# Optimization experiments

Measured on AMD Instinct MI355X. Metric: run time of the kernel, lower is better.

## Reference

```python
import jax, jax.numpy as jnp
import numpy as np

B, D, H, T = 4096, 512, 1024, 20
DT = 0.05  # time spacing for the integration grid


def setup_inputs() -> dict:
    key = jax.random.key(0)
    k1, k2, k3 = jax.random.split(key, 3)
    x0 = jax.random.normal(k1, (B, D), dtype=jnp.float32)
    t = jnp.arange(T, dtype=jnp.float32) * DT  # monotonically increasing time grid
    W1 = jax.random.normal(k2, (D, H), dtype=jnp.float32) * (1.0 / np.sqrt(D))
    b1 = jnp.zeros((H,), dtype=jnp.float32)
    W2 = jax.random.normal(k3, (H, D), dtype=jnp.float32) * (1.0 / np.sqrt(H))
    b2 = jnp.zeros((D,), dtype=jnp.float32)
    return {"x0": x0, "t": t, "W1": W1, "b1": b1, "W2": W2, "b2": b2}


def reference(x0, t, W1, b1, W2, b2):
    """NeuralODE forward: integrate dy/dt = f(t, y) from x0 over grid t.

    f is the canonical 2-layer tanh MLP odefunc (autonomous in t, as in the
    typical odefunc(input_dim) construction). Integration uses classic RK4 on
    the supplied time grid (fixed-grid equivalent of odeint). Returns the
    trajectory with shape [T, B, D], matching torchdiffeq's odeint output.
    """

    def f(ti, y):  # odefunc: [B, D] -> [B, D]
        return jnp.tanh(y @ W1 + b1) @ W2 + b2

    def rk4_step(y, td):
        ti, dt = td
        half = dt * 0.5
        k1 = f(ti, y)
        k2 = f(ti + half, y + half * k1)
        k3 = f(ti + half, y + half * k2)
        k4 = f(ti + dt, y + dt * k3)
        y_next = y + (dt / 6.0) * (k1 + 2.0 * k2 + 2.0 * k3 + k4)
        return y_next, y_next

    dts = t[1:] - t[:-1]  # [T-1]
    _, ys = jax.lax.scan(rk4_step, x0, (t[:-1], dts))  # ys: [T-1, B, D]
    return jnp.concatenate([x0[None], ys], axis=0)  # [T, B, D]
```

## Files before the change

kernel.cpp:

```cpp
#include <hip/hip_runtime.h>
#include <hip/hip_bf16.h>
#include <cstdint>

#define BATCH 4096
#define DIM   512
#define HID   1024
#define TSTEPS 20

typedef unsigned short u16;
typedef short s16x8 __attribute__((ext_vector_type(8)));
typedef float f32x4 __attribute__((ext_vector_type(4)));

__device__ __forceinline__ u16 f2bf(float f) {
    unsigned int u = __float_as_uint(f);
    u = (u + 0x7FFFu + ((u >> 16) & 1u)) >> 16;
    return (u16)u;
}

__global__ void init_state(const float* __restrict__ x0, float* __restrict__ out0,
                           u16* __restrict__ ybf, int n) {
    int i = blockIdx.x * blockDim.x + threadIdx.x;
    if (i < n) { float v = x0[i]; out0[i] = v; ybf[i] = f2bf(v); }
}

__global__ void transpose_convert(const float* __restrict__ W, u16* __restrict__ Wt,
                                  int K, int N) {
    int n = blockIdx.x * 32 + threadIdx.x;
    int k = blockIdx.y * 8  + threadIdx.y;
    if (n < N && k < K) Wt[(size_t)n * K + k] = f2bf(W[(size_t)k * N + n]);
}

template<int BM, int BN, int EPI>
__global__ __launch_bounds__(256, 2) void gemm_bt(
    const u16* __restrict__ A,
    const u16* __restrict__ Bt,
    const float* __restrict__ bias,
    int M, int N, int K,
    u16* __restrict__ actOut,
    const float* __restrict__ ybase,
    float* __restrict__ ynext,
    float* __restrict__ accum,
    u16* __restrict__ ybf,
    const float* __restrict__ tgrid, int step)
{
    constexpr int AC = BM / 8;
    constexpr int BC = BN / 8;
    constexpr int CPW = (AC + BC) / 4;
    static_assert(CPW == 4 || CPW == 6, "vmcnt literals below assume 4 or 6");
    constexpr int WM = BM / 32;
    constexpr int WN = BN / 32;
    constexpr int BUFE = (BM + BN) * 64;

    __shared__ u16 lds[3 * BUFE];

    const int tid  = threadIdx.x;
    const int lane = tid & 63;
    const int wid  = tid >> 6;
    const int wy   = wid >> 1;
    const int wx   = wid & 1;
    const int brow = blockIdx.x * BM;
    const int bcol = blockIdx.y * BN;

    const int srow = lane >> 3;
    const int scol = ((lane & 7) ^ srow) * 8;

    f32x4 acc[WM][WN];
#pragma unroll
    for (int m = 0; m < WM; ++m)
#pragma unroll
        for (int n = 0; n < WN; ++n)
            acc[m][n] = (f32x4){0.f, 0.f, 0.f, 0.f};

    auto stage = [&](int buf, int kt) {
        const int k0 = kt * 64;
        u16* base = &lds[buf * BUFE];
#pragma unroll
        for (int c0 = 0; c0 < CPW; ++c0) {
            int c = wid * CPW + c0;
            if (c < AC) {
                int row = c * 8 + srow;
                const u16* g = A + (size_t)(brow + row) * K + k0 + scol;
                __builtin_amdgcn_global_load_lds(
                    (const __attribute__((address_space(1))) unsigned int*)g,
                    (__attribute__((address_space(3))) unsigned int*)&base[c * 512],
                    16, 0, 0);
            } else {
                int cb = c - AC;
                int row = cb * 8 + srow;
                const u16* g = Bt + (size_t)(bcol + row) * K + k0 + scol;
                __builtin_amdgcn_global_load_lds(
                    (const __attribute__((address_space(1))) unsigned int*)g,
                    (__attribute__((address_space(3))) unsigned int*)&base[BM * 64 + cb * 512],
                    16, 0, 0);
            }
        }
    };

    const int NT = K / 64;

    stage(0, 0);
    stage(1, 1);

    for (int kt = 0; kt < NT; ++kt) {
        if (kt < NT - 1) {
            if constexpr (CPW == 6) asm volatile("s_waitcnt vmcnt(6)" ::: "memory");
            else                    asm volatile("s_waitcnt vmcnt(4)" ::: "memory");
        } else {
            asm volatile("s_waitcnt vmcnt(0)" ::: "memory");
        }
        __builtin_amdgcn_s_barrier();

        const char* lb = (const char*)&lds[(kt % 3) * BUFE];

        s16x8 af[2][WM], bfr[2][WN];
#pragma unroll
        for (int ks = 0; ks < 2; ++ks) {
#pragma unroll
            for (int m = 0; m < WM; ++m) {
                int row = wy * (BM / 2) + m * 16 + (lane & 15);
                unsigned byte = (unsigned)(row * 128 + (ks * 32 + (lane >> 4) * 8) * 2);
                byte ^= (unsigned)((row & 7) << 4);
                af[ks][m] = *(const s16x8*)(lb + byte);
            }
#pragma unroll
            for (int n = 0; n < WN; ++n) {
                int row = wx * (BN / 2) + n * 16 + (lane & 15);
                unsigned byte = (unsigned)(BM * 128 + row * 128 + (ks * 32 + (lane >> 4) * 8) * 2);
                byte ^= (unsigned)((row & 7) << 4);
                bfr[ks][n] = *(const s16x8*)(lb + byte);
            }
        }

        if (kt + 2 < NT) stage((kt + 2) % 3, kt + 2);

#pragma unroll
        for (int ks = 0; ks < 2; ++ks)
#pragma unroll
            for (int m = 0; m < WM; ++m)
#pragma unroll
                for (int n = 0; n < WN; ++n)
                    acc[m][n] = __builtin_amdgcn_mfma_f32_16x16x32_bf16(
                        af[ks][m], bfr[ks][n], acc[m][n], 0, 0, 0);

        __builtin_amdgcn_s_barrier();
    }

    float dtv = 0.f;
    if constexpr (EPI >= 1) dtv = tgrid[step + 1] - tgrid[step];

#pragma unroll
    for (int m = 0; m < WM; ++m) {
        int row0 = brow + wy * (BM / 2) + m * 16 + (lane >> 4) * 4;
#pragma unroll
        for (int n = 0; n < WN; ++n) {
            int col = bcol + wx * (BN / 2) + n * 16 + (lane & 15);
            float bv = bias[col];
#pragma unroll
            for (int j = 0; j < 4; ++j) {
                int row = row0 + j;
                float v = acc[m][n][j] + bv;
                if constexpr (EPI == 0) {
                    actOut[(size_t)row * HID + col] = f2bf(tanhf(v));
                } else {
                    size_t idx = (size_t)row * DIM + col;
                    float yb = ybase[idx];
                    if constexpr (EPI == 1) {
                        accum[idx] = v;
                        ybf[idx] = f2bf(yb + 0.5f * dtv * v);
                    } else if constexpr (EPI == 2) {
                        accum[idx] += 2.0f * v;
                        ybf[idx] = f2bf(yb + 0.5f * dtv * v);
                    } else if constexpr (EPI == 3) {
                        accum[idx] += 2.0f * v;
                        ybf[idx] = f2bf(yb + dtv * v);
                    } else {
                        float yn = yb + (dtv * (1.0f / 6.0f)) * (accum[idx] + v);
                        ynext[idx] = yn;
                        ybf[idx] = f2bf(yn);
                    }
                }
            }
        }
    }
}

extern "C" void kernel_launch(void* const* d_in, const int* in_sizes, int n_in,
                              void* d_out, int out_size, void* d_ws, size_t ws_size,
                              hipStream_t stream) {
    (void)in_sizes; (void)n_in; (void)out_size; (void)ws_size;
    const float* x0 = (const float*)d_in[0];
    const float* t  = (const float*)d_in[1];
    const float* W1 = (const float*)d_in[2];
    const float* b1 = (const float*)d_in[3];
    const float* W2 = (const float*)d_in[4];
    const float* b2 = (const float*)d_in[5];
    float* out = (float*)d_out;

    char* ws = (char*)d_ws;
    u16*   ybf   = (u16*)  (ws);
    u16*   act   = (u16*)  (ws + (4u  << 20));
    float* accum = (float*)(ws + (12u << 20));
    u16*   W1T   = (u16*)  (ws + (20u << 20));
    u16*   W2T   = (u16*)  (ws + (21u << 20));

    init_state<<<(BATCH * DIM + 255) / 256, 256, 0, stream>>>(x0, out, ybf, BATCH * DIM);
    transpose_convert<<<dim3(HID / 32, DIM / 8), dim3(32, 8), 0, stream>>>(W1, W1T, DIM, HID);
    transpose_convert<<<dim3(DIM / 32, HID / 8), dim3(32, 8), 0, stream>>>(W2, W2T, HID, DIM);

    dim3 blk(256);
    dim3 g1(BATCH / 128, HID / 64);
    dim3 g2(BATCH / 64,  DIM / 64);

    for (int s = 0; s < TSTEPS - 1; ++s) {
        const float* yb_s = out + (size_t)s * BATCH * DIM;
        float*       yn_s = out + (size_t)(s + 1) * BATCH * DIM;

        gemm_bt<128,64,0><<<g1, blk, 0, stream>>>(ybf, W1T, b1, BATCH, HID, DIM,
                                                  act, nullptr, nullptr, nullptr, nullptr, nullptr, 0);
        gemm_bt<64,64,1><<<g2, blk, 0, stream>>>(act, W2T, b2, BATCH, DIM, HID,
                                                 nullptr, yb_s, yn_s, accum, ybf, t, s);
        gemm_bt<128,64,0><<<g1, blk, 0, stream>>>(ybf, W1T, b1, BATCH, HID, DIM,
                                                  act, nullptr, nullptr, nullptr, nullptr, nullptr, 0);
        gemm_bt<64,64,2><<<g2, blk, 0, stream>>>(act, W2T, b2, BATCH, DIM, HID,
                                                 nullptr, yb_s, yn_s, accum, ybf, t, s);
        gemm_bt<128,64,0><<<g1, blk, 0, stream>>>(ybf, W1T, b1, BATCH, HID, DIM,
                                                  act, nullptr, nullptr, nullptr, nullptr, nullptr, 0);
        gemm_bt<64,64,3><<<g2, blk, 0, stream>>>(act, W2T, b2, BATCH, DIM, HID,
                                                 nullptr, yb_s, yn_s, accum, ybf, t, s);
        gemm_bt<128,64,0><<<g1, blk, 0, stream>>>(ybf, W1T, b1, BATCH, HID, DIM,
                                                  act, nullptr, nullptr, nullptr, nullptr, nullptr, 0);
        gemm_bt<64,64,4><<<g2, blk, 0, stream>>>(act, W2T, b2, BATCH, DIM, HID,
                                                 nullptr, yb_s, yn_s, accum, ybf, t, s);
    }
}
```

Measured before the change: 2.020 ms.

## Deepen W2 GEMM prefetch, drop trailing barrier, use fast tanh

Parameterizes the GEMM's async LDS prefetch depth, using a 3-stage lookahead with 4 buffers for the second-layer GEMM and keeping depth 2 for the first. It removes the end-of-iteration barrier, relying on the buffer ring so that the slot being refilled was last read before the top barrier. It also replaces tanhf in the hidden-layer epilogue with an exp/rcp based approximation. The cost is more LDS per block for the W2 GEMM and slightly lower tanh accuracy.

```diff
diff --git a/kernel.cpp b/kernel.cpp
--- a/kernel.cpp
+++ b/kernel.cpp
@@ -15,6 +15,13 @@
     unsigned int u = __float_as_uint(f);
     u = (u + 0x7FFFu + ((u >> 16) & 1u)) >> 16;
     return (u16)u;
+}
+
+__device__ __forceinline__ float fast_tanh(float x) {
+    float ax = __builtin_fabsf(x);
+    float e  = __expf(2.0f * ax);
+    float t  = 1.0f - 2.0f * __builtin_amdgcn_rcpf(e + 1.0f);
+    return __builtin_copysignf(t, x);
 }
 
 __global__ void init_state(const float* __restrict__ x0, float* __restrict__ out0,
@@ -30,7 +37,7 @@
     if (n < N && k < K) Wt[(size_t)n * K + k] = f2bf(W[(size_t)k * N + n]);
 }
 
-template<int BM, int BN, int EPI>
+template<int BM, int BN, int EPI, int DEPTH>
 __global__ __launch_bounds__(256, 2) void gemm_bt(
     const u16* __restrict__ A,
     const u16* __restrict__ Bt,
@@ -46,12 +53,14 @@
     constexpr int AC = BM / 8;
     constexpr int BC = BN / 8;
     constexpr int CPW = (AC + BC) / 4;
-    static_assert(CPW == 4 || CPW == 6, "vmcnt literals below assume 4 or 6");
+    constexpr int NBUF = DEPTH + 1;
+    static_assert((DEPTH == 2 && CPW == 6) || (DEPTH == 3 && CPW == 4),
+                  "vmcnt literals below assume these configs");
     constexpr int WM = BM / 32;
     constexpr int WN = BN / 32;
     constexpr int BUFE = (BM + BN) * 64;
 
-    __shared__ u16 lds[3 * BUFE];
+    __shared__ u16 lds[NBUF * BUFE];
 
     const int tid  = threadIdx.x;
     const int lane = tid & 63;
@@ -98,19 +107,21 @@
 
     const int NT = K / 64;
 
-    stage(0, 0);
-    stage(1, 1);
+#pragma unroll
+    for (int d = 0; d < DEPTH; ++d) stage(d, d);
 
     for (int kt = 0; kt < NT; ++kt) {
-        if (kt < NT - 1) {
-            if constexpr (CPW == 6) asm volatile("s_waitcnt vmcnt(6)" ::: "memory");
-            else                    asm volatile("s_waitcnt vmcnt(4)" ::: "memory");
+        if constexpr (DEPTH == 2) {
+            if (kt < NT - 1) asm volatile("s_waitcnt vmcnt(6)" ::: "memory");
+            else             asm volatile("s_waitcnt vmcnt(0)" ::: "memory");
         } else {
-            asm volatile("s_waitcnt vmcnt(0)" ::: "memory");
+            if (kt < NT - 2)       asm volatile("s_waitcnt vmcnt(8)" ::: "memory");
+            else if (kt == NT - 2) asm volatile("s_waitcnt vmcnt(4)" ::: "memory");
+            else                   asm volatile("s_waitcnt vmcnt(0)" ::: "memory");
         }
         __builtin_amdgcn_s_barrier();
 
-        const char* lb = (const char*)&lds[(kt % 3) * BUFE];
+        const char* lb = (const char*)&lds[(kt % NBUF) * BUFE];
 
         s16x8 af[2][WM], bfr[2][WN];
 #pragma unroll
@@ -131,7 +142,7 @@
             }
         }
 
-        if (kt + 2 < NT) stage((kt + 2) % 3, kt + 2);
+        if (kt + DEPTH < NT) stage((kt + DEPTH) % NBUF, kt + DEPTH);
 
 #pragma unroll
         for (int ks = 0; ks < 2; ++ks)
@@ -141,8 +152,6 @@
                 for (int n = 0; n < WN; ++n)
                     acc[m][n] = __builtin_amdgcn_mfma_f32_16x16x32_bf16(
                         af[ks][m], bfr[ks][n], acc[m][n], 0, 0, 0);
-
-        __builtin_amdgcn_s_barrier();
     }
 
     float dtv = 0.f;
@@ -160,7 +169,7 @@
                 int row = row0 + j;
                 float v = acc[m][n][j] + bv;
                 if constexpr (EPI == 0) {
-                    actOut[(size_t)row * HID + col] = f2bf(tanhf(v));
+                    actOut[(size_t)row * HID + col] = f2bf(fast_tanh(v));
                 } else {
                     size_t idx = (size_t)row * DIM + col;
                     float yb = ybase[idx];
@@ -215,21 +224,21 @@
         const float* yb_s = out + (size_t)s * BATCH * DIM;
         float*       yn_s = out + (size_t)(s + 1) * BATCH * DIM;
 
-        gemm_bt<128,64,0><<<g1, blk, 0, stream>>>(ybf, W1T, b1, BATCH, HID, DIM,
-                                                  act, nullptr, nullptr, nullptr, nullptr, nullptr, 0);
-        gemm_bt<64,64,1><<<g2, blk, 0, stream>>>(act, W2T, b2, BATCH, DIM, HID,
-                                                 nullptr, yb_s, yn_s, accum, ybf, t, s);
-        gemm_bt<128,64,0><<<g1, blk, 0, stream>>>(ybf, W1T, b1, BATCH, HID, DIM,
-                                                  act, nullptr, nullptr, nullptr, nullptr, nullptr, 0);
-        gemm_bt<64,64,2><<<g2, blk, 0, stream>>>(act, W2T, b2, BATCH, DIM, HID,
-                                                 nullptr, yb_s, yn_s, accum, ybf, t, s);
-        gemm_bt<128,64,0><<<g1, blk, 0, stream>>>(ybf, W1T, b1, BATCH, HID, DIM,
-                                                  act, nullptr, nullptr, nullptr, nullptr, nullptr, 0);
-        gemm_bt<64,64,3><<<g2, blk, 0, stream>>>(act, W2T, b2, BATCH, DIM, HID,
-                                                 nullptr, yb_s, yn_s, accum, ybf, t, s);
-        gemm_bt<128,64,0><<<g1, blk, 0, stream>>>(ybf, W1T, b1, BATCH, HID, DIM,
-                                                  act, nullptr, nullptr, nullptr, nullptr, nullptr, 0);
-        gemm_bt<64,64,4><<<g2, blk, 0, stream>>>(act, W2T, b2, BATCH, DIM, HID,
-                                                 nullptr, yb_s, yn_s, accum, ybf, t, s);
+        gemm_bt<128,64,0,2><<<g1, blk, 0, stream>>>(ybf, W1T, b1, BATCH, HID, DIM,
+                                                    act, nullptr, nullptr, nullptr, nullptr, nullptr, 0);
+        gemm_bt<64,64,1,3><<<g2, blk, 0, stream>>>(act, W2T, b2, BATCH, DIM, HID,
+                                                   nullptr, yb_s, yn_s, accum, ybf, t, s);
+        gemm_bt<128,64,0,2><<<g1, blk, 0, stream>>>(ybf, W1T, b1, BATCH, HID, DIM,
+                                                    act, nullptr, nullptr, nullptr, nullptr, nullptr, 0);
+        gemm_bt<64,64,2,3><<<g2, blk, 0, stream>>>(act, W2T, b2, BATCH, DIM, HID,
+                                                   nullptr, yb_s, yn_s, accum, ybf, t, s);
+        gemm_bt<128,64,0,2><<<g1, blk, 0, stream>>>(ybf, W1T, b1, BATCH, HID, DIM,
+                                                    act, nullptr, nullptr, nullptr, nullptr, nullptr, 0);
+        gemm_bt<64,64,3,3><<<g2, blk, 0, stream>>>(act, W2T, b2, BATCH, DIM, HID,
+                                                   nullptr, yb_s, yn_s, accum, ybf, t, s);
+        gemm_bt<128,64,0,2><<<g1, blk, 0, stream>>>(ybf, W1T, b1, BATCH, HID, DIM,
+                                                    act, nullptr, nullptr, nullptr, nullptr, nullptr, 0);
+        gemm_bt<64,64,4,3><<<g2, blk, 0, stream>>>(act, W2T, b2, BATCH, DIM, HID,
+                                                   nullptr, yb_s, yn_s, accum, ybf, t, s);
     }
 }
```

Result: faster. 1.755 ms (-13.2%).
